# Kernel optimization log

Measured on AMD Instinct MI355X. Metric: run time of the kernel, lower is better.

## Reference

```python
import jax, jax.numpy as jnp
import numpy as np

T, B, M = 2048, 256, 32


def setup_inputs() -> dict:
    key = jax.random.key(0)
    k1, k2, k3, k4 = jax.random.split(key, 4)
    emissions = jax.random.normal(k1, (T, B, M), jnp.float32)
    tags = jax.random.randint(k2, (T, B), 0, M)
    # weight divides transition scores -> keep strictly positive
    weight = jax.random.uniform(k3, (T, B), jnp.float32, 0.5, 1.5)
    mask = jnp.ones((T, B), jnp.int32)  # first timestep must be all-on
    transitions = jax.random.normal(k4, (M, M), jnp.float32) * 0.1
    start_transitions = jnp.zeros((M,), jnp.float32)
    end_transitions = jnp.zeros((M,), jnp.float32)
    return {
        "emissions": emissions,
        "tags": tags,
        "weight": weight,
        "mask": mask,
        "transitions": transitions,
        "start_transitions": start_transitions,
        "end_transitions": end_transitions,
    }


def reference(emissions, tags, weight, mask, transitions, start_transitions, end_transitions):
    # emissions: [T,B,M]; tags/weight/mask: [T,B]; reduction='sum' (torch default)
    Tn, Bn, Mn = emissions.shape
    maskb = mask.astype(bool)
    tags = jnp.where(maskb, tags, 1)
    maskf = mask.astype(emissions.dtype)

    # ---- gold-path score (_compute_score) ----
    score = start_transitions[tags[0]]
    score = score + (transitions[tags[:-1], tags[1:]] * maskf[1:] / weight[:-1]).sum(0)
    em_sc = jnp.take_along_axis(emissions, tags[:, :, None], axis=-1)[..., 0] * maskf
    score = score + em_sc.sum(0)
    seq_ends = mask.astype(jnp.int32).sum(0) - 1  # [B]
    last_tags = tags[seq_ends, jnp.arange(Bn)]
    score = score + end_transitions[last_tags]

    # ---- log-partition (_compute_normalizer) via logsumexp-semiring scan ----
    neg_inf = jnp.asarray(-jnp.inf, emissions.dtype)
    log_eye = jnp.where(jnp.eye(Mn, dtype=bool), jnp.zeros((), emissions.dtype), neg_inf)

    alpha0 = start_transitions + emissions[0]  # [B,M]

    def step(alpha, xs):
        em_t, w_t, m_t = xs  # [B,M], [B], [B]
        sc = transitions[None, :, :] / w_t[:, None, None] + em_t[:, None, :]  # [B,M,M]
        sc = jnp.where(m_t[:, None, None], sc, log_eye)  # masked step = identity in log-semiring
        alpha = jax.nn.logsumexp(alpha[:, :, None] + sc, axis=1)
        return alpha, None

    alpha, _ = jax.lax.scan(step, alpha0, (emissions[1:], weight[:-1], maskb[1:]))
    log_Z = jax.nn.logsumexp(alpha + end_transitions, axis=1)  # [B]

    nllh = log_Z - score
    return nllh.sum()
```

## Files before the change

kernel.cpp:

```cpp
#include <hip/hip_runtime.h>
#include <hip/hip_bf16.h>
#include <stdint.h>


#define T_DIM 2048
#define B_DIM 256
#define M_DIM 32
#define CHUNKS 32
#define CLEN 64
#define NBLK ((CHUNKS * B_DIM) / 16)
#define KSC 184.6649652337873f
#define SBIAS2 12599160.66f

typedef __attribute__((ext_vector_type(8))) short short8;
typedef __attribute__((ext_vector_type(16))) float f32x16;

__device__ __forceinline__ int pack_bf16(float lo, float hi) {
  union { float f; uint32_t u; } a, b;
  a.f = lo; b.f = hi;
  return (int)__builtin_amdgcn_perm(b.u, a.u, 0x07060302u);
}

__device__ __forceinline__ int pack_lo16(int lo, int hi) {
  return (int)__builtin_amdgcn_perm((uint32_t)hi, (uint32_t)lo, 0x05040100u);
}

__device__ __forceinline__ float bcast_lane(float v, int idx) {
  return __int_as_float(__builtin_amdgcn_readlane(__float_as_int(v), idx));
}

__global__ __launch_bounds__(256, 2) void chunk_kernel(
    const float* __restrict__ em, const int* __restrict__ tags,
    const float* __restrict__ wt, const int* __restrict__ mask,
    const float* __restrict__ trans, const float* __restrict__ endt,
    uint32_t* __restrict__ mats, float* __restrict__ offs,
    float* __restrict__ scoreP, uint32_t* __restrict__ ctrl)
{
  int tid = threadIdx.x;
  if (tid == 0) ctrl[0] = 0;
  int lane = tid & 63;
  int h = lane >> 5;
  int r = lane & 31;
  int wid = blockIdx.x * 4 + (tid >> 6);
  int u0 = 4 * wid;
  int bb = u0 & (B_DIM - 1);
  int c = u0 >> 8;
  int t0 = 1 + c * CLEN;
  int t1 = t0 + CLEN; if (t1 > T_DIM) t1 = T_DIM;

  float tpre[16];
#pragma unroll
  for (int j = 0; j < 8; ++j) {
    int row = ((j < 4) ? j : j + 4) + 4 * h;
    tpre[j]     = trans[row * 32 + r] * KSC;
    tpre[8 + j] = trans[(row + 16) * 32 + r] * KSC;
  }

  int tw = t0 - 1 + lane; if (tw > T_DIM - 1) tw = T_DIM - 1;
  int tmk = t0 + lane; if (tmk > T_DIM - 1) tmk = T_DIM - 1;
  float rwv[4];
  uint64_t mk[4];
  uint64_t valid = (t1 - t0 >= 64) ? ~0ull : ((1ull << (t1 - t0)) - 1ull);
#pragma unroll
  for (int ch = 0; ch < 4; ++ch) {
    rwv[ch] = __builtin_amdgcn_rcpf(wt[tw * B_DIM + bb + ch]);
    mk[ch] = __ballot(mask[tmk * B_DIM + bb + ch] != 0) & valid;
  }

  f32x16 X[4];
#pragma unroll
  for (int p = 0; p < 16; ++p) {
    float v = (((p & 3) + 8 * (p >> 2) + 4 * h) == r) ? 1.f : 0.f;
    X[0][p] = v; X[1][p] = v; X[2][p] = v; X[3][p] = v;
  }
  f32x16 z;
#pragma unroll
  for (int u = 0; u < 16; ++u) z[u] = 0.f;

  float off2[4] = {0.f, 0.f, 0.f, 0.f};

  auto step4 = [&](const float* e4, int s) {
    float rw0 = bcast_lane(rwv[0], s), rw1 = bcast_lane(rwv[1], s);
    float rw2 = bcast_lane(rwv[2], s), rw3 = bcast_lane(rwv[3], s);
    float rw[4] = {rw0, rw1, rw2, rw3};
    union { int i[4]; short8 s8; } af1[4], af2[4], b1[4], b2[4];
#pragma unroll
    for (int ch = 0; ch < 4; ++ch) {
      float e = fmaf(e4[ch], KSC, SBIAS2);
      float qf[16];
#pragma unroll
      for (int j = 0; j < 16; ++j)
        qf[j] = fmaf(tpre[j], rw[ch], e);
#pragma unroll
      for (int u = 0; u < 4; ++u) {
        af1[ch].i[u] = pack_lo16(__float_as_int(qf[2 * u]),     __float_as_int(qf[2 * u + 1]));
        af2[ch].i[u] = pack_lo16(__float_as_int(qf[8 + 2 * u]), __float_as_int(qf[8 + 2 * u + 1]));
      }
    }
#pragma unroll
    for (int ch = 0; ch < 4; ++ch)
#pragma unroll
      for (int u = 0; u < 4; ++u) {
        b1[ch].i[u] = pack_bf16(X[ch][2 * u],     X[ch][2 * u + 1]);
        b2[ch].i[u] = pack_bf16(X[ch][8 + 2 * u], X[ch][8 + 2 * u + 1]);
      }
    f32x16 d[4];
#pragma unroll
    for (int ch = 0; ch < 4; ++ch)
      d[ch] = __builtin_amdgcn_mfma_f32_32x32x16_bf16(af1[ch].s8, b1[ch].s8, z, 0, 0, 0);
#pragma unroll
    for (int ch = 0; ch < 4; ++ch)
      X[ch] = __builtin_amdgcn_mfma_f32_32x32x16_bf16(af2[ch].s8, b2[ch].s8, d[ch], 0, 0, 0);
  };

  auto stepOne = [&](f32x16& Xc, float e_em, float rw) {
    float e = fmaf(e_em, KSC, SBIAS2);
    float qf[16];
#pragma unroll
    for (int j = 0; j < 16; ++j)
      qf[j] = fmaf(tpre[j], rw, e);
    union { int i[4]; short8 s8; } af1, af2, b1_, b2_;
#pragma unroll
    for (int u = 0; u < 4; ++u) {
      af1.i[u] = pack_lo16(__float_as_int(qf[2 * u]),     __float_as_int(qf[2 * u + 1]));
      af2.i[u] = pack_lo16(__float_as_int(qf[8 + 2 * u]), __float_as_int(qf[8 + 2 * u + 1]));
      b1_.i[u] = pack_bf16(Xc[2 * u],     Xc[2 * u + 1]);
      b2_.i[u] = pack_bf16(Xc[8 + 2 * u], Xc[8 + 2 * u + 1]);
    }
    f32x16 d = __builtin_amdgcn_mfma_f32_32x32x16_bf16(af1.s8, b1_.s8, z, 0, 0, 0);
    Xc = __builtin_amdgcn_mfma_f32_32x32x16_bf16(af2.s8, b2_.s8, d, 0, 0, 0);
  };

  auto rescale = [&](f32x16& Xc, float& o2) {
    float mx = Xc[0];
#pragma unroll
    for (int u = 1; u < 16; ++u) mx = fmaxf(mx, Xc[u]);
#pragma unroll
    for (int off = 1; off < 64; off <<= 1) mx = fmaxf(mx, __shfl_xor(mx, off));
    float sc = __builtin_amdgcn_rcpf(mx);
    o2 += __builtin_amdgcn_logf(mx);
#pragma unroll
    for (int u = 0; u < 16; ++u) Xc[u] *= sc;
  };

  bool fast = (t1 - t0 == 64) && (mk[0] == ~0ull) && (mk[1] == ~0ull)
            && (mk[2] == ~0ull) && (mk[3] == ~0ull);

  if (fast) {
    float e[4][4], n[4][4];
#pragma unroll
    for (int ch = 0; ch < 4; ++ch)
#pragma unroll
      for (int u = 0; u < 4; ++u)
        e[ch][u] = em[((size_t)((t0 + 2 * u + h) * B_DIM + bb + ch)) * 32 + r];
    for (int g = 0; g < 8; ++g) {
      int tg = t0 + 8 * (g + 1);
#pragma unroll
      for (int ch = 0; ch < 4; ++ch)
#pragma unroll
        for (int u = 0; u < 4; ++u) {
          int tt = tg + 2 * u + h; if (tt > T_DIM - 1) tt = T_DIM - 1;
          n[ch][u] = em[((size_t)(tt * B_DIM + bb + ch)) * 32 + r];
        }
#pragma unroll
      for (int u = 0; u < 4; ++u) {
        int sA = 8 * g + 2 * u, sB = sA + 1;
        float eA[4], eB[4];
#pragma unroll
        for (int ch = 0; ch < 4; ++ch) {
          float sw = __shfl_xor(e[ch][u], 32);
          eA[ch] = h ? sw : e[ch][u];
          eB[ch] = h ? e[ch][u] : sw;
        }
        step4(eA, sA);
        step4(eB, sB);
      }
#pragma unroll
      for (int ch = 0; ch < 4; ++ch) rescale(X[ch], off2[ch]);
#pragma unroll
      for (int ch = 0; ch < 4; ++ch)
#pragma unroll
        for (int u = 0; u < 4; ++u) e[ch][u] = n[ch][u];
    }
  } else {
    float emv[4], emp[4];
#pragma unroll
    for (int ch = 0; ch < 4; ++ch)
      emv[ch] = em[((size_t)((t0 + h) * B_DIM + bb + ch)) * 32 + r];
    int tpf = t0 + 2 + h; if (tpf > T_DIM - 1) tpf = T_DIM - 1;
#pragma unroll
    for (int ch = 0; ch < 4; ++ch)
      emp[ch] = em[((size_t)(tpf * B_DIM + bb + ch)) * 32 + r];

    for (int it = 0; it < CLEN / 2; ++it) {
      int tn = t0 + 2 * it + 4 + h; if (tn > T_DIM - 1) tn = T_DIM - 1;
      float emn[4];
#pragma unroll
      for (int ch = 0; ch < 4; ++ch)
        emn[ch] = em[((size_t)(tn * B_DIM + bb + ch)) * 32 + r];

      int sA = 2 * it, sB = sA + 1;
#pragma unroll
      for (int ch = 0; ch < 4; ++ch) {
        float sw = __shfl_xor(emv[ch], 32);
        if ((mk[ch] >> sA) & 1)
          stepOne(X[ch], h ? sw : emv[ch], bcast_lane(rwv[ch], sA));
        if ((t0 + sB < t1) && ((mk[ch] >> sB) & 1))
          stepOne(X[ch], h ? emv[ch] : sw, bcast_lane(rwv[ch], sB));
      }

      if ((it & 3) == 3) {
#pragma unroll
        for (int ch = 0; ch < 4; ++ch) rescale(X[ch], off2[ch]);
      }
#pragma unroll
      for (int ch = 0; ch < 4; ++ch) { emv[ch] = emp[ch]; emp[ch] = emn[ch]; }
    }
  }

#pragma unroll
  for (int ch = 0; ch < 4; ++ch) {
    uint32_t* mp = mats + (size_t)(u0 + ch) * 512;
#pragma unroll
    for (int u = 0; u < 8; ++u) {
      int pairIdx = (u & 1) + (u >> 1) * 4 + 2 * h;
      mp[pairIdx * 32 + r] = (uint32_t)pack_bf16(X[ch][2 * u], X[ch][2 * u + 1]);
    }
  }
  if (lane == 0) {
#pragma unroll
    for (int ch = 0; ch < 4; ++ch) offs[u0 + ch] = off2[ch];
  }

  int t = t0 + lane;
  float ssc = 0.f;
  if (t < t1) {
#pragma unroll
    for (int ch = 0; ch < 4; ++ch) {
      int b = bb + ch;
      int mkc  = mask[t * B_DIM + b];
      int mkn  = (t + 1 < T_DIM) ? mask[(t + 1) * B_DIM + b] : 0;
      int tg   = mkc ? tags[t * B_DIM + b] : 1;
      int mkp  = mask[(t - 1) * B_DIM + b];
      int tgp  = mkp ? tags[(t - 1) * B_DIM + b] : 1;
      if (mkc)
        ssc += em[(size_t)(t * B_DIM + b) * 32 + tg]
             + trans[tgp * 32 + tg] * __builtin_amdgcn_rcpf(wt[(t - 1) * B_DIM + b]);
      if (mkc && !mkn) ssc += endt[tg];
    }
  }
#pragma unroll
  for (int off = 32; off; off >>= 1) ssc += __shfl_xor(ssc, off);
  if (lane == 0) scoreP[wid] = -ssc;
}

__global__ __launch_bounds__(64) void combine_kernel(
    const float* __restrict__ em, const int* __restrict__ tags,
    const int* __restrict__ mask, const float* __restrict__ startt,
    const float* __restrict__ endt, const uint32_t* __restrict__ mats,
    const float* __restrict__ offs, const float* __restrict__ scoreP,
    float* __restrict__ res, uint32_t* __restrict__ ctrl,
    float* __restrict__ out)
{
  const float INV_LN2 = 1.44269504088896340736f;
  const float LN2 = 0.69314718055994530942f;
  int lane = threadIdx.x;
  int j = lane & 31;
  int h = lane >> 5;
  int b = blockIdx.x;
  int jp = j >> 1, jh = j & 1;

  float a0 = (startt[j] + em[(size_t)b * 32 + j]) * INV_LN2;
  float c0 = a0;
#pragma unroll
  for (int off = 1; off < 32; off <<= 1) c0 = fmaxf(c0, __shfl_xor(c0, off));
  float av = __builtin_amdgcn_exp2f(a0 - c0);
  float acc = c0;

  const uint4* xr0 = (const uint4*)(mats + (size_t)b * 512 + jp * 32 + 16 * h);
  uint4 nv0 = xr0[0], nv1 = xr0[1];
  float noff = offs[b];

  for (int c = 0; c < CHUNKS; ++c) {
    uint4 v0 = nv0, v1 = nv1;
    float offc = noff;
    int cn = (c + 1 < CHUNKS) ? c + 1 : c;
    const uint4* xrn = (const uint4*)(mats + (size_t)(cn * B_DIM + b) * 512 + jp * 32 + 16 * h);
    nv0 = xrn[0]; nv1 = xrn[1];
    noff = offs[cn * B_DIM + b];

    float x[8];
    uint32_t u0[4] = {v0.x, v0.y, v0.z, v0.w};
    uint32_t u1[4] = {v1.x, v1.y, v1.z, v1.w};
#pragma unroll
    for (int e = 0; e < 4; ++e) {
      uint32_t bits0 = jh ? (u0[e] & 0xFFFF0000u) : (u0[e] << 16);
      uint32_t bits1 = jh ? (u1[e] & 0xFFFF0000u) : (u1[e] << 16);
      union { uint32_t uu; float f; } cv0, cv1;
      cv0.uu = bits0; cv1.uu = bits1;
      x[e] = cv0.f; x[4 + e] = cv1.f;
    }
    float s0 = 0.f, s1 = 0.f;
#pragma unroll
    for (int i = 0; i < 4; ++i) {
      s0 = fmaf(x[i],     __shfl(av, 16 * h + i),     s0);
      s1 = fmaf(x[4 + i], __shfl(av, 16 * h + 4 + i), s1);
    }
    float an = s0 + s1;
    an += __shfl_xor(an, 32);
    float mx = an;
#pragma unroll
    for (int off = 1; off < 32; off <<= 1) mx = fmaxf(mx, __shfl_xor(mx, off));
    av = an * __builtin_amdgcn_rcpf(mx);
    acc += __builtin_amdgcn_logf(mx) + offc;
  }

  float sv = av * __builtin_amdgcn_exp2f(endt[j] * INV_LN2);
#pragma unroll
  for (int off = 1; off < 32; off <<= 1) sv += __shfl_xor(sv, off);
  if (lane == 0) {
    float logZ = (acc + __builtin_amdgcn_logf(sv)) * LN2;
    int mk0 = mask[b];
    int tg0 = mk0 ? tags[b] : 1;
    float s0 = startt[tg0] + (mk0 ? em[(size_t)b * 32 + tg0] : 0.f);
    int mk1 = mask[B_DIM + b];
    if (mk0 && !mk1) s0 += endt[tg0];
    res[b] = logZ - s0;
  }

  __builtin_amdgcn_fence(__ATOMIC_RELEASE, "agent");
  unsigned old = 0;
  if (lane == 0) old = atomicAdd(&ctrl[0], 1u);
  old = (unsigned)__shfl((int)old, 0);
  if (old == (unsigned)(B_DIM - 1)) {
    __builtin_amdgcn_fence(__ATOMIC_ACQUIRE, "agent");
    float s = 0.f;
#pragma unroll
    for (int i = 0; i < 4; ++i) s += res[lane + 64 * i];
#pragma unroll
    for (int i = 0; i < 32; ++i) s += scoreP[lane + 64 * i];
#pragma unroll
    for (int off = 32; off; off >>= 1) s += __shfl_xor(s, off);
    if (lane == 0) out[0] = s;
  }
}

extern "C" void kernel_launch(void* const* d_in, const int* in_sizes, int n_in,
                              void* d_out, int out_size, void* d_ws, size_t ws_size,
                              hipStream_t stream) {
  const float* em   = (const float*)d_in[0];
  const int*   tags = (const int*)d_in[1];
  const float* wt   = (const float*)d_in[2];
  const int*   mask = (const int*)d_in[3];
  const float* tr   = (const float*)d_in[4];
  const float* stt  = (const float*)d_in[5];
  const float* ent  = (const float*)d_in[6];
  float* out = (float*)d_out;

  uint32_t* ctrl  = (uint32_t*)d_ws;
  float* res      = (float*)d_ws + 4;
  float* scoreP   = res + B_DIM;
  float* offs     = scoreP + 4 * NBLK;
  uint32_t* mats  = (uint32_t*)(offs + CHUNKS * B_DIM);

  chunk_kernel<<<NBLK, 256, 0, stream>>>(em, tags, wt, mask, tr, ent,
                                         mats, offs, scoreP, ctrl);
  combine_kernel<<<B_DIM, 64, 0, stream>>>(em, tags, mask, stt, ent,
                                           mats, offs, scoreP, res, ctrl, out);
}
```

Before: 177.2 us.

## Parallelize chunk-matrix combine with MFMA tree reduction across four waves

The combine kernel previously walked all 32 chunk transfer matrices serially, one vector-matrix product per chunk in a single wave. Each block now uses four waves, and each wave multiplies eight chunk matrices together with bf16 MFMA. Each wave normalizes its product and writes it to LDS, then one wave applies the four partial products to the initial alpha vector. This shortens the serial dependency chain in the combine stage, at the cost of an extra bf16 rounding of intermediate matrix products and more threads per block.

```diff
diff --git a/kernel.cpp b/kernel.cpp
--- a/kernel.cpp
+++ b/kernel.cpp
@@ -254,7 +254,7 @@
   if (lane == 0) scoreP[wid] = -ssc;
 }
 
-__global__ __launch_bounds__(64) void combine_kernel(
+__global__ __launch_bounds__(256, 1) void combine_kernel(
     const float* __restrict__ em, const int* __restrict__ tags,
     const int* __restrict__ mask, const float* __restrict__ startt,
     const float* __restrict__ endt, const uint32_t* __restrict__ mats,
@@ -264,55 +264,112 @@
 {
   const float INV_LN2 = 1.44269504088896340736f;
   const float LN2 = 0.69314718055994530942f;
-  int lane = threadIdx.x;
-  int j = lane & 31;
+  __shared__ float Plds[4][32][36];
+  __shared__ float logw[4];
+
+  int tid = threadIdx.x;
+  int lane = tid & 63;
+  int w = tid >> 6;
+  int r = lane & 31;
   int h = lane >> 5;
   int b = blockIdx.x;
-  int jp = j >> 1, jh = j & 1;
-
+
+  uint32_t rsel = (r & 1) ? 0x07060302u : 0x05040100u;
+  int rowoff = (r >> 1) * 32;
+
+  f32x16 P, z;
+#pragma unroll
+  for (int p = 0; p < 16; ++p) {
+    P[p] = ((((p & 3) + 8 * (p >> 2) + 4 * h) == r) ? 1.f : 0.f);
+    z[p] = 0.f;
+  }
+
+  int c0 = 8 * w;
+  uint4 L[4][4];
+#pragma unroll
+  for (int i = 0; i < 4; ++i) {
+    const uint4* mb = (const uint4*)(mats + ((size_t)(c0 + i) * B_DIM + b) * 512 + rowoff);
+    L[i][0] = mb[h]; L[i][1] = mb[2 + h]; L[i][2] = mb[4 + h]; L[i][3] = mb[6 + h];
+  }
+
+  float lw = 0.f;
+#pragma unroll
+  for (int i = 0; i < 8; ++i) {
+    uint4 A0 = L[i & 3][0], A1 = L[i & 3][1], A2 = L[i & 3][2], A3 = L[i & 3][3];
+    if (i + 4 < 8) {
+      const uint4* mb = (const uint4*)(mats + ((size_t)(c0 + i + 4) * B_DIM + b) * 512 + rowoff);
+      L[i & 3][0] = mb[h]; L[i & 3][1] = mb[2 + h];
+      L[i & 3][2] = mb[4 + h]; L[i & 3][3] = mb[6 + h];
+    }
+    union { int i4[4]; short8 s8; } af1, af2, b1, b2;
+    af1.i4[0] = (int)__builtin_amdgcn_perm(A0.y, A0.x, rsel);
+    af1.i4[1] = (int)__builtin_amdgcn_perm(A0.w, A0.z, rsel);
+    af1.i4[2] = (int)__builtin_amdgcn_perm(A1.y, A1.x, rsel);
+    af1.i4[3] = (int)__builtin_amdgcn_perm(A1.w, A1.z, rsel);
+    af2.i4[0] = (int)__builtin_amdgcn_perm(A2.y, A2.x, rsel);
+    af2.i4[1] = (int)__builtin_amdgcn_perm(A2.w, A2.z, rsel);
+    af2.i4[2] = (int)__builtin_amdgcn_perm(A3.y, A3.x, rsel);
+    af2.i4[3] = (int)__builtin_amdgcn_perm(A3.w, A3.z, rsel);
+#pragma unroll
+    for (int u = 0; u < 4; ++u) {
+      b1.i4[u] = pack_bf16(P[2 * u],     P[2 * u + 1]);
+      b2.i4[u] = pack_bf16(P[8 + 2 * u], P[8 + 2 * u + 1]);
+    }
+    f32x16 d = __builtin_amdgcn_mfma_f32_32x32x16_bf16(af1.s8, b1.s8, z, 0, 0, 0);
+    P = __builtin_amdgcn_mfma_f32_32x32x16_bf16(af2.s8, b2.s8, d, 0, 0, 0);
+    lw += offs[(size_t)(c0 + i) * B_DIM + b];
+  }
+
+  float mx = P[0];
+#pragma unroll
+  for (int p = 1; p < 16; ++p) mx = fmaxf(mx, P[p]);
+#pragma unroll
+  for (int off = 1; off < 64; off <<= 1) mx = fmaxf(mx, __shfl_xor(mx, off));
+  float sc = __builtin_amdgcn_rcpf(mx);
+  lw += __builtin_amdgcn_logf(mx);
+#pragma unroll
+  for (int p = 0; p < 16; ++p)
+    Plds[w][(p & 3) + 8 * (p >> 2) + 4 * h][r] = P[p] * sc;
+  if (lane == 0) logw[w] = lw;
+  __syncthreads();
+
+  if (tid >= 64) return;
+
+  int j = r;
   float a0 = (startt[j] + em[(size_t)b * 32 + j]) * INV_LN2;
-  float c0 = a0;
-#pragma unroll
-  for (int off = 1; off < 32; off <<= 1) c0 = fmaxf(c0, __shfl_xor(c0, off));
-  float av = __builtin_amdgcn_exp2f(a0 - c0);
-  float acc = c0;
-
-  const uint4* xr0 = (const uint4*)(mats + (size_t)b * 512 + jp * 32 + 16 * h);
-  uint4 nv0 = xr0[0], nv1 = xr0[1];
-  float noff = offs[b];
-
-  for (int c = 0; c < CHUNKS; ++c) {
-    uint4 v0 = nv0, v1 = nv1;
-    float offc = noff;
-    int cn = (c + 1 < CHUNKS) ? c + 1 : c;
-    const uint4* xrn = (const uint4*)(mats + (size_t)(cn * B_DIM + b) * 512 + jp * 32 + 16 * h);
-    nv0 = xrn[0]; nv1 = xrn[1];
-    noff = offs[cn * B_DIM + b];
-
-    float x[8];
-    uint32_t u0[4] = {v0.x, v0.y, v0.z, v0.w};
-    uint32_t u1[4] = {v1.x, v1.y, v1.z, v1.w};
-#pragma unroll
-    for (int e = 0; e < 4; ++e) {
-      uint32_t bits0 = jh ? (u0[e] & 0xFFFF0000u) : (u0[e] << 16);
-      uint32_t bits1 = jh ? (u1[e] & 0xFFFF0000u) : (u1[e] << 16);
-      union { uint32_t uu; float f; } cv0, cv1;
-      cv0.uu = bits0; cv1.uu = bits1;
-      x[e] = cv0.f; x[4 + e] = cv1.f;
-    }
-    float s0 = 0.f, s1 = 0.f;
-#pragma unroll
-    for (int i = 0; i < 4; ++i) {
-      s0 = fmaf(x[i],     __shfl(av, 16 * h + i),     s0);
-      s1 = fmaf(x[4 + i], __shfl(av, 16 * h + 4 + i), s1);
-    }
-    float an = s0 + s1;
-    an += __shfl_xor(an, 32);
-    float mx = an;
-#pragma unroll
-    for (int off = 1; off < 32; off <<= 1) mx = fmaxf(mx, __shfl_xor(mx, off));
-    av = an * __builtin_amdgcn_rcpf(mx);
-    acc += __builtin_amdgcn_logf(mx) + offc;
+  float cm = a0;
+#pragma unroll
+  for (int off = 1; off < 32; off <<= 1) cm = fmaxf(cm, __shfl_xor(cm, off));
+  float av = __builtin_amdgcn_exp2f(a0 - cm);
+  float acc = cm + logw[0] + logw[1] + logw[2] + logw[3];
+
+#pragma unroll
+  for (int wv = 0; wv < 4; ++wv) {
+    const float4* Pr = (const float4*)&Plds[wv][j][16 * h];
+    float4 q0 = Pr[0], q1 = Pr[1], q2 = Pr[2], q3 = Pr[3];
+    int cb = 16 * h;
+    float s = fmaf(q0.x, __shfl(av, cb + 0),
+              fmaf(q0.y, __shfl(av, cb + 1),
+              fmaf(q0.z, __shfl(av, cb + 2),
+                   q0.w * __shfl(av, cb + 3))));
+    s = fmaf(q1.x, __shfl(av, cb + 4),
+        fmaf(q1.y, __shfl(av, cb + 5),
+        fmaf(q1.z, __shfl(av, cb + 6),
+        fmaf(q1.w, __shfl(av, cb + 7), s))));
+    s = fmaf(q2.x, __shfl(av, cb + 8),
+        fmaf(q2.y, __shfl(av, cb + 9),
+        fmaf(q2.z, __shfl(av, cb + 10),
+        fmaf(q2.w, __shfl(av, cb + 11), s))));
+    s = fmaf(q3.x, __shfl(av, cb + 12),
+        fmaf(q3.y, __shfl(av, cb + 13),
+        fmaf(q3.z, __shfl(av, cb + 14),
+        fmaf(q3.w, __shfl(av, cb + 15), s))));
+    float an = s + __shfl_xor(s, 32);
+    float m2 = an;
+#pragma unroll
+    for (int off = 1; off < 32; off <<= 1) m2 = fmaxf(m2, __shfl_xor(m2, off));
+    av = an * __builtin_amdgcn_rcpf(m2);
+    acc += __builtin_amdgcn_logf(m2);
   }
 
   float sv = av * __builtin_amdgcn_exp2f(endt[j] * INV_LN2);
@@ -334,14 +391,14 @@
   old = (unsigned)__shfl((int)old, 0);
   if (old == (unsigned)(B_DIM - 1)) {
     __builtin_amdgcn_fence(__ATOMIC_ACQUIRE, "agent");
-    float s = 0.f;
-#pragma unroll
-    for (int i = 0; i < 4; ++i) s += res[lane + 64 * i];
-#pragma unroll
-    for (int i = 0; i < 32; ++i) s += scoreP[lane + 64 * i];
-#pragma unroll
-    for (int off = 32; off; off >>= 1) s += __shfl_xor(s, off);
-    if (lane == 0) out[0] = s;
+    float sfin = 0.f;
+#pragma unroll
+    for (int i = 0; i < 4; ++i) sfin += res[lane + 64 * i];
+#pragma unroll
+    for (int i = 0; i < 32; ++i) sfin += scoreP[lane + 64 * i];
+#pragma unroll
+    for (int off = 32; off; off >>= 1) sfin += __shfl_xor(sfin, off);
+    if (lane == 0) out[0] = sfin;
   }
 }
 
@@ -365,6 +422,6 @@
 
   chunk_kernel<<<NBLK, 256, 0, stream>>>(em, tags, wt, mask, tr, ent,
                                          mats, offs, scoreP, ctrl);
-  combine_kernel<<<B_DIM, 64, 0, stream>>>(em, tags, mask, stt, ent,
-                                           mats, offs, scoreP, res, ctrl, out);
-}
+  combine_kernel<<<B_DIM, 256, 0, stream>>>(em, tags, mask, stt, ent,
+                                            mats, offs, scoreP, res, ctrl, out);
+}
```

Result: faster. 169.2 us (-4.5%).

## Fuse chunk combine into chunk kernel via last-block MFMA matrix product

Applied to the files above, without the earlier changes.

Removes the separate combine kernel. The last block to finish in each of 16 groups now chains the 32 chunk transfer matrices for its batch columns using bf16 MFMA matrix-matrix products, with periodic rescaling. A second atomic counter picks one block to do the final sum. A tiny zero kernel clears the counters before the main kernel. This removes a launch and the per-batch serial matrix-vector chain, but it puts a serial tail on 16 blocks and adds matrix-matrix work in bf16, which may cost precision.

```diff
diff --git a/kernel.cpp b/kernel.cpp
--- a/kernel.cpp
+++ b/kernel.cpp
@@ -29,15 +29,24 @@
   return __int_as_float(__builtin_amdgcn_readlane(__float_as_int(v), idx));
 }
 
+__global__ void zero_kernel(uint32_t* __restrict__ ctrl) {
+  if (threadIdx.x < 32) ctrl[threadIdx.x] = 0;
+}
+
 __global__ __launch_bounds__(256, 2) void chunk_kernel(
     const float* __restrict__ em, const int* __restrict__ tags,
     const float* __restrict__ wt, const int* __restrict__ mask,
-    const float* __restrict__ trans, const float* __restrict__ endt,
+    const float* __restrict__ trans, const float* __restrict__ startt,
+    const float* __restrict__ endt,
     uint32_t* __restrict__ mats, float* __restrict__ offs,
-    float* __restrict__ scoreP, uint32_t* __restrict__ ctrl)
+    float* __restrict__ scoreP, float* __restrict__ res,
+    uint32_t* __restrict__ ctrl, float* __restrict__ out)
 {
+  const float INV_LN2 = 1.44269504088896340736f;
+  const float LN2 = 0.69314718055994530942f;
+  __shared__ unsigned sOld;
+
   int tid = threadIdx.x;
-  if (tid == 0) ctrl[0] = 0;
   int lane = tid & 63;
   int h = lane >> 5;
   int r = lane & 31;
@@ -252,96 +261,111 @@
 #pragma unroll
   for (int off = 32; off; off >>= 1) ssc += __shfl_xor(ssc, off);
   if (lane == 0) scoreP[wid] = -ssc;
-}
-
-__global__ __launch_bounds__(64) void combine_kernel(
-    const float* __restrict__ em, const int* __restrict__ tags,
-    const int* __restrict__ mask, const float* __restrict__ startt,
-    const float* __restrict__ endt, const uint32_t* __restrict__ mats,
-    const float* __restrict__ offs, const float* __restrict__ scoreP,
-    float* __restrict__ res, uint32_t* __restrict__ ctrl,
-    float* __restrict__ out)
-{
-  const float INV_LN2 = 1.44269504088896340736f;
-  const float LN2 = 0.69314718055994530942f;
-  int lane = threadIdx.x;
-  int j = lane & 31;
-  int h = lane >> 5;
-  int b = blockIdx.x;
-  int jp = j >> 1, jh = j & 1;
-
-  float a0 = (startt[j] + em[(size_t)b * 32 + j]) * INV_LN2;
-  float c0 = a0;
-#pragma unroll
-  for (int off = 1; off < 32; off <<= 1) c0 = fmaxf(c0, __shfl_xor(c0, off));
-  float av = __builtin_amdgcn_exp2f(a0 - c0);
-  float acc = c0;
-
-  const uint4* xr0 = (const uint4*)(mats + (size_t)b * 512 + jp * 32 + 16 * h);
-  uint4 nv0 = xr0[0], nv1 = xr0[1];
-  float noff = offs[b];
-
-  for (int c = 0; c < CHUNKS; ++c) {
-    uint4 v0 = nv0, v1 = nv1;
-    float offc = noff;
-    int cn = (c + 1 < CHUNKS) ? c + 1 : c;
-    const uint4* xrn = (const uint4*)(mats + (size_t)(cn * B_DIM + b) * 512 + jp * 32 + 16 * h);
-    nv0 = xrn[0]; nv1 = xrn[1];
-    noff = offs[cn * B_DIM + b];
-
-    float x[8];
-    uint32_t u0[4] = {v0.x, v0.y, v0.z, v0.w};
-    uint32_t u1[4] = {v1.x, v1.y, v1.z, v1.w};
-#pragma unroll
-    for (int e = 0; e < 4; ++e) {
-      uint32_t bits0 = jh ? (u0[e] & 0xFFFF0000u) : (u0[e] << 16);
-      uint32_t bits1 = jh ? (u1[e] & 0xFFFF0000u) : (u1[e] << 16);
-      union { uint32_t uu; float f; } cv0, cv1;
-      cv0.uu = bits0; cv1.uu = bits1;
-      x[e] = cv0.f; x[4 + e] = cv1.f;
-    }
-    float s0 = 0.f, s1 = 0.f;
-#pragma unroll
-    for (int i = 0; i < 4; ++i) {
-      s0 = fmaf(x[i],     __shfl(av, 16 * h + i),     s0);
-      s1 = fmaf(x[4 + i], __shfl(av, 16 * h + 4 + i), s1);
-    }
-    float an = s0 + s1;
-    an += __shfl_xor(an, 32);
-    float mx = an;
-#pragma unroll
-    for (int off = 1; off < 32; off <<= 1) mx = fmaxf(mx, __shfl_xor(mx, off));
-    av = an * __builtin_amdgcn_rcpf(mx);
-    acc += __builtin_amdgcn_logf(mx) + offc;
-  }
-
-  float sv = av * __builtin_amdgcn_exp2f(endt[j] * INV_LN2);
-#pragma unroll
-  for (int off = 1; off < 32; off <<= 1) sv += __shfl_xor(sv, off);
-  if (lane == 0) {
-    float logZ = (acc + __builtin_amdgcn_logf(sv)) * LN2;
-    int mk0 = mask[b];
-    int tg0 = mk0 ? tags[b] : 1;
-    float s0 = startt[tg0] + (mk0 ? em[(size_t)b * 32 + tg0] : 0.f);
-    int mk1 = mask[B_DIM + b];
-    if (mk0 && !mk1) s0 += endt[tg0];
-    res[b] = logZ - s0;
-  }
-
-  __builtin_amdgcn_fence(__ATOMIC_RELEASE, "agent");
-  unsigned old = 0;
-  if (lane == 0) old = atomicAdd(&ctrl[0], 1u);
-  old = (unsigned)__shfl((int)old, 0);
-  if (old == (unsigned)(B_DIM - 1)) {
-    __builtin_amdgcn_fence(__ATOMIC_ACQUIRE, "agent");
-    float s = 0.f;
-#pragma unroll
-    for (int i = 0; i < 4; ++i) s += res[lane + 64 * i];
-#pragma unroll
-    for (int i = 0; i < 32; ++i) s += scoreP[lane + 64 * i];
-#pragma unroll
-    for (int off = 32; off; off >>= 1) s += __shfl_xor(s, off);
-    if (lane == 0) out[0] = s;
+
+  __syncthreads();
+  int grp = blockIdx.x & 15;
+  if (tid == 0) {
+    __builtin_amdgcn_fence(__ATOMIC_RELEASE, "agent");
+    sOld = atomicAdd(&ctrl[grp], 1u);
+  }
+  __syncthreads();
+  if (sOld != 31u) return;
+  __builtin_amdgcn_fence(__ATOMIC_ACQUIRE, "agent");
+
+  {
+    uint32_t rsel = (r & 1) ? 0x07060302u : 0x05040100u;
+    int rowoff = (r >> 1) * 32;
+    f32x16 P[4];
+#pragma unroll
+    for (int p = 0; p < 16; ++p) {
+      float v = (((p & 3) + 8 * (p >> 2) + 4 * h) == r) ? 1.f : 0.f;
+      P[0][p] = v; P[1][p] = v; P[2][p] = v; P[3][p] = v;
+    }
+    float lwc[4] = {0.f, 0.f, 0.f, 0.f};
+
+#pragma unroll 2
+    for (int cc = 0; cc < CHUNKS; ++cc) {
+      uint4 A[4][4];
+#pragma unroll
+      for (int ch = 0; ch < 4; ++ch) {
+        const uint4* mb = (const uint4*)(mats + ((size_t)(cc * B_DIM + bb + ch)) * 512 + rowoff);
+        A[ch][0] = mb[h]; A[ch][1] = mb[2 + h];
+        A[ch][2] = mb[4 + h]; A[ch][3] = mb[6 + h];
+        lwc[ch] += offs[(size_t)cc * B_DIM + bb + ch];
+      }
+#pragma unroll
+      for (int ch = 0; ch < 4; ++ch) {
+        union { int i4[4]; short8 s8; } af1, af2, b1, b2;
+        af1.i4[0] = (int)__builtin_amdgcn_perm(A[ch][0].y, A[ch][0].x, rsel);
+        af1.i4[1] = (int)__builtin_amdgcn_perm(A[ch][0].w, A[ch][0].z, rsel);
+        af1.i4[2] = (int)__builtin_amdgcn_perm(A[ch][1].y, A[ch][1].x, rsel);
+        af1.i4[3] = (int)__builtin_amdgcn_perm(A[ch][1].w, A[ch][1].z, rsel);
+        af2.i4[0] = (int)__builtin_amdgcn_perm(A[ch][2].y, A[ch][2].x, rsel);
+        af2.i4[1] = (int)__builtin_amdgcn_perm(A[ch][2].w, A[ch][2].z, rsel);
+        af2.i4[2] = (int)__builtin_amdgcn_perm(A[ch][3].y, A[ch][3].x, rsel);
+        af2.i4[3] = (int)__builtin_amdgcn_perm(A[ch][3].w, A[ch][3].z, rsel);
+#pragma unroll
+        for (int u = 0; u < 4; ++u) {
+          b1.i4[u] = pack_bf16(P[ch][2 * u],     P[ch][2 * u + 1]);
+          b2.i4[u] = pack_bf16(P[ch][8 + 2 * u], P[ch][8 + 2 * u + 1]);
+        }
+        f32x16 d = __builtin_amdgcn_mfma_f32_32x32x16_bf16(af1.s8, b1.s8, z, 0, 0, 0);
+        P[ch] = __builtin_amdgcn_mfma_f32_32x32x16_bf16(af2.s8, b2.s8, d, 0, 0, 0);
+      }
+      if ((cc & 7) == 7) {
+#pragma unroll
+        for (int ch = 0; ch < 4; ++ch) rescale(P[ch], lwc[ch]);
+      }
+    }
+
+    float ee[16];
+#pragma unroll
+    for (int p = 0; p < 16; ++p)
+      ee[p] = __builtin_amdgcn_exp2f(endt[(p & 3) + 8 * (p >> 2) + 4 * h] * INV_LN2);
+
+#pragma unroll
+    for (int ch = 0; ch < 4; ++ch) {
+      int b = bb + ch;
+      float a0 = (startt[r] + em[(size_t)b * 32 + r]) * INV_LN2;
+      float cm = a0;
+#pragma unroll
+      for (int off = 1; off < 32; off <<= 1) cm = fmaxf(cm, __shfl_xor(cm, off));
+      float av = __builtin_amdgcn_exp2f(a0 - cm);
+      float s = 0.f;
+#pragma unroll
+      for (int p = 0; p < 16; ++p) s = fmaf(P[ch][p], ee[p], s);
+      s *= av;
+#pragma unroll
+      for (int off = 1; off < 64; off <<= 1) s += __shfl_xor(s, off);
+      if (lane == 0) {
+        float logZ = (cm + lwc[ch] + __builtin_amdgcn_logf(s)) * LN2;
+        int mk0 = mask[b];
+        int tg0 = mk0 ? tags[b] : 1;
+        float s0 = startt[tg0] + (mk0 ? em[(size_t)b * 32 + tg0] : 0.f);
+        int mk1 = mask[B_DIM + b];
+        if (mk0 && !mk1) s0 += endt[tg0];
+        res[b] = logZ - s0;
+      }
+    }
+  }
+
+  __syncthreads();
+  if (tid == 0) {
+    __builtin_amdgcn_fence(__ATOMIC_RELEASE, "agent");
+    sOld = atomicAdd(&ctrl[16], 1u);
+  }
+  __syncthreads();
+  if (sOld != 15u) return;
+  __builtin_amdgcn_fence(__ATOMIC_ACQUIRE, "agent");
+  if (tid < 64) {
+    float sfin = 0.f;
+#pragma unroll
+    for (int i = 0; i < 4; ++i) sfin += res[lane + 64 * i];
+#pragma unroll
+    for (int i = 0; i < 32; ++i) sfin += scoreP[lane + 64 * i];
+#pragma unroll
+    for (int off = 32; off; off >>= 1) sfin += __shfl_xor(sfin, off);
+    if (lane == 0) out[0] = sfin;
   }
 }
 
@@ -358,13 +382,12 @@
   float* out = (float*)d_out;
 
   uint32_t* ctrl  = (uint32_t*)d_ws;
-  float* res      = (float*)d_ws + 4;
+  float* res      = (float*)d_ws + 32;
   float* scoreP   = res + B_DIM;
   float* offs     = scoreP + 4 * NBLK;
   uint32_t* mats  = (uint32_t*)(offs + CHUNKS * B_DIM);
 
-  chunk_kernel<<<NBLK, 256, 0, stream>>>(em, tags, wt, mask, tr, ent,
-                                         mats, offs, scoreP, ctrl);
-  combine_kernel<<<B_DIM, 64, 0, stream>>>(em, tags, mask, stt, ent,
-                                           mats, offs, scoreP, res, ctrl, out);
-}
+  zero_kernel<<<1, 64, 0, stream>>>(ctrl);
+  chunk_kernel<<<NBLK, 256, 0, stream>>>(em, tags, wt, mask, tr, stt, ent,
+                                         mats, offs, scoreP, res, ctrl, out);
+}
```

Result: slower. 199.7 us (+12.7%).
